# Performance work log

Hardware: AMD Instinct MI355X
Metric: run time of the kernel (lower is better)

## Reference

```python
import math
import jax, jax.numpy as jnp
import numpy as np

B, N, D_FULL, M, D_V = 8, 4096, 256, 256, 256


def _phi(x, omega):
    # x: [..., N, d_full], omega: [M, d_full] -> [..., N, M]
    proj = x @ omega.T
    log_phi = proj - 0.5 * jnp.sum(x * x, axis=-1, keepdims=True)
    log_phi = log_phi - jnp.max(log_phi, axis=-1, keepdims=True)
    return jnp.exp(log_phi) / math.sqrt(omega.shape[0])


def _causal(phi_q, phi_k, V):
    # phi_q/phi_k: [B, N, M], V: [B, N, d_v]
    b, n, m = phi_q.shape
    d_v = V.shape[-1]

    def step(carry, inp):
        S, z = carry
        pq, pk, v = inp  # [B,M], [B,M], [B,d_v]
        S = S + pk[:, :, None] * v[:, None, :]          # [B, M, d_v]
        z = z + pk                                       # [B, M]
        num = jnp.einsum('bi,bij->bj', pq, S)            # [B, d_v]
        den = jnp.maximum(jnp.sum(pq * z, axis=-1), 1e-6)
        return (S, z), num / den[:, None]

    S0 = jnp.zeros((b, m, d_v), phi_q.dtype)
    z0 = jnp.zeros((b, m), phi_q.dtype)
    xs = (jnp.swapaxes(phi_q, 0, 1), jnp.swapaxes(phi_k, 0, 1), jnp.swapaxes(V, 0, 1))
    _, ys = jax.lax.scan(step, (S0, z0), xs)  # ys: [N, B, d_v]
    return jnp.swapaxes(ys, 0, 1)


def setup_inputs() -> dict:
    key = jax.random.key(0)
    kq, kk, kv, ko = jax.random.split(key, 4)
    Q = jax.random.normal(kq, (B, N, D_FULL), dtype=jnp.float32)
    K_in = jax.random.normal(kk, (B, N, D_FULL), dtype=jnp.float32)
    V = jax.random.normal(kv, (B, N, D_V), dtype=jnp.float32)
    omega = jax.random.normal(ko, (M, D_FULL), dtype=jnp.float32)
    return {"Q": Q, "K_in": K_in, "V": V, "omega": omega, "causal": 1}


def reference(Q, K_in, V, omega, causal):
    phi_q = _phi(Q, omega)
    phi_k = _phi(K_in, omega)
    if causal:
        return _causal(phi_q, phi_k, V)
    S = jnp.einsum('bni,bnj->bij', phi_k, V)          # [B, M, d_v]
    z = jnp.sum(phi_k, axis=-2)                        # [B, M]
    num = jnp.einsum('bni,bij->bnj', phi_q, S)
    den = jnp.maximum(jnp.einsum('bni,bi->bn', phi_q, z), 1e-6)
    return num / den[..., None]
```

## Files before the change

### kernel.cpp

```cpp
#include <hip/hip_runtime.h>

#define BN 8
#define NN 4096
#define DD 256
#define MM 256
#define DV 256
#define CHUNK 256
#define NC (NN / CHUNK)

using f32x4 = __attribute__((ext_vector_type(4))) float;
using s16x8 = __attribute__((ext_vector_type(8))) short;

#define MFMA16(a, b, c) __builtin_amdgcn_mfma_f32_16x16x32_bf16(a, b, c, 0, 0, 0)

__device__ __forceinline__ unsigned short f2bf(float x) {
    union { float f; unsigned int u; } v; v.f = x;
    unsigned int r = v.u + 0x7FFF + ((v.u >> 16) & 1);
    return (unsigned short)(r >> 16);
}
__device__ __forceinline__ float bf2f(unsigned short u) {
    union { unsigned int u; float f; } v; v.u = ((unsigned int)u) << 16;
    return v.f;
}

__global__ __launch_bounds__(256) void omconv(
    const float* __restrict__ Om, unsigned short* __restrict__ OmH,
    unsigned short* __restrict__ OmL)
{
    const int i = blockIdx.x * 256 + threadIdx.x;
    const float4 v = *(const float4*)(Om + (size_t)i * 4);
    const float xs[4] = {v.x, v.y, v.z, v.w};
    unsigned short h[4], l[4];
#pragma unroll
    for (int j = 0; j < 4; ++j) {
        h[j] = f2bf(xs[j]);
        l[j] = f2bf(xs[j] - bf2f(h[j]));
    }
    *(uint2*)(OmH + (size_t)i * 4) = *(uint2*)h;
    *(uint2*)(OmL + (size_t)i * 4) = *(uint2*)l;
}

template<bool KPATH>
__global__ __launch_bounds__(256) void phi_mfma(
    const float* __restrict__ X, const unsigned short* __restrict__ OmH,
    const unsigned short* __restrict__ OmL, unsigned short* __restrict__ Phi,
    unsigned short* __restrict__ PhiT, float* __restrict__ Zp)
{
    const int tid = threadIdx.x;
    const int w = tid >> 6;
    const int lane = tid & 63;
    const int col = lane & 15, quad = lane >> 4;
    const long r0 = (long)blockIdx.x * 64;

    __shared__ __align__(16) char lds[67584];
    __shared__ float rowmax_s[64];
    short (*Xh)[264] = (short(*)[264])lds;
    short (*Xl)[264] = (short(*)[264])(lds + 33792);
    unsigned short (*P)[264] = (unsigned short(*)[264])lds;
    unsigned int* P32 = (unsigned int*)lds;
    float (*red)[67] = (float(*)[67])(lds + 34048);

    float4 xv[16];
#pragma unroll
    for (int i = 0; i < 16; ++i)
        xv[i] = *(const float4*)(X + r0 * DD + (size_t)(i * 256 + tid) * 4);
#pragma unroll
    for (int i = 0; i < 16; ++i) {
        const int f = i * 256 + tid;
        const int row = f >> 6;
        const int k4 = (f & 63) * 4;
        const float xs[4] = {xv[i].x, xv[i].y, xv[i].z, xv[i].w};
        unsigned short hh[4], ll[4];
#pragma unroll
        for (int j = 0; j < 4; ++j) {
            hh[j] = f2bf(xs[j]);
            ll[j] = f2bf(xs[j] - bf2f(hh[j]));
        }
        *(uint2*)&Xh[row][k4] = *(uint2*)hh;
        *(uint2*)&Xl[row][k4] = *(uint2*)ll;
    }
    __syncthreads();

    f32x4 acc[4][4] = {};
    s16x8 bh0[4], bl0[4], bh1[4], bl1[4];
#pragma unroll
    for (int ct = 0; ct < 4; ++ct) {
        const size_t off = (size_t)(w * 64 + ct * 16 + col) * DD + quad * 8;
        bh0[ct] = *(const s16x8*)(OmH + off);
        bl0[ct] = *(const s16x8*)(OmL + off);
    }
#pragma unroll
    for (int kt = 0; kt < 8; ++kt) {
        if (kt < 7) {
#pragma unroll
            for (int ct = 0; ct < 4; ++ct) {
                const size_t off = (size_t)(w * 64 + ct * 16 + col) * DD + (kt + 1) * 32 + quad * 8;
                bh1[ct] = *(const s16x8*)(OmH + off);
                bl1[ct] = *(const s16x8*)(OmL + off);
            }
        }
        s16x8 ah[4], al[4];
#pragma unroll
        for (int t = 0; t < 4; ++t) {
            ah[t] = *(const s16x8*)&Xh[t * 16 + col][kt * 32 + quad * 8];
            al[t] = *(const s16x8*)&Xl[t * 16 + col][kt * 32 + quad * 8];
        }
#pragma unroll
        for (int t = 0; t < 4; ++t)
#pragma unroll
            for (int ct = 0; ct < 4; ++ct) {
                acc[t][ct] = MFMA16(ah[t], bh0[ct], acc[t][ct]);
                acc[t][ct] = MFMA16(ah[t], bl0[ct], acc[t][ct]);
                acc[t][ct] = MFMA16(al[t], bh0[ct], acc[t][ct]);
            }
#pragma unroll
        for (int ct = 0; ct < 4; ++ct) { bh0[ct] = bh1[ct]; bl0[ct] = bl1[ct]; }
    }

    __syncthreads();
#pragma unroll
    for (int t = 0; t < 4; ++t)
#pragma unroll
        for (int r = 0; r < 4; ++r) {
            float m = acc[t][0][r];
#pragma unroll
            for (int ct = 1; ct < 4; ++ct) m = fmaxf(m, acc[t][ct][r]);
            red[t * 16 + quad * 4 + r][w * 16 + col] = m;
        }
    __syncthreads();
    if (tid < 64) {
        float m = red[tid][0];
#pragma unroll
        for (int j = 1; j < 64; ++j) m = fmaxf(m, red[tid][j]);
        rowmax_s[tid] = m;
    }
    __syncthreads();

#pragma unroll
    for (int t = 0; t < 4; ++t)
#pragma unroll
        for (int r = 0; r < 4; ++r) {
            const int n = t * 16 + quad * 4 + r;
            const float rm = rowmax_s[n];
#pragma unroll
            for (int ct = 0; ct < 4; ++ct) {
                const float val = __expf(acc[t][ct][r] - rm) * 0.0625f;
                const unsigned u = (unsigned)f2bf(val);
                const unsigned up = (unsigned)__shfl_xor((int)u, 1);
                if ((col & 1) == 0)
                    P32[n * 132 + w * 32 + ct * 8 + (col >> 1)] = u | (up << 16);
            }
        }
    __syncthreads();

    {
        const int t7 = tid & 7;
        const int nb = tid >> 3;
#pragma unroll
        for (int p2 = 0; p2 < 2; ++p2) {
            const int n = p2 * 32 + nb;
#pragma unroll
            for (int s = 0; s < 4; ++s)
                *(uint4*)(Phi + (r0 + n) * MM + t7 * 8 + s * 64) =
                    *(const uint4*)&P[n][t7 * 8 + s * 64];
        }
    }

    if (KPATH) {
        const int b = blockIdx.x >> 6;
        const int c = (blockIdx.x >> 2) & 15;
        const int n0 = (int)(r0 & (NN - 1));
        const int m0 = tid & 31;
        const int nsub = tid >> 5;
#pragma unroll
        for (int mi = 0; mi < 8; ++mi) {
            const int m = mi * 32 + m0;
            unsigned short u[8];
#pragma unroll
            for (int j = 0; j < 8; ++j) u[j] = P[nsub * 8 + j][m];
            *(uint4*)(PhiT + ((size_t)b * MM + m) * NN + n0 + nsub * 8) = *(uint4*)u;
        }
        float z = 0.f;
#pragma unroll
        for (int n = 0; n < 64; ++n) z += bf2f(P[n][tid]);
        atomicAdd(&Zp[((b * NC + c) << 8) + tid], z);
    }
}

__global__ __launch_bounds__(256) void transpose_v(
    const float* __restrict__ V, unsigned short* __restrict__ VT)
{
    const int tid = threadIdx.x;
    const int ct = blockIdx.x & 3;
    const long r0 = (long)(blockIdx.x >> 2) * 64;
    const int b = (int)(r0 >> 12);
    const int n0 = (int)(r0 & (NN - 1));
    __shared__ unsigned short T[64][72];
    const int rr = tid >> 4, cs = tid & 15;
#pragma unroll
    for (int p = 0; p < 4; ++p) {
        const int r = p * 16 + rr;
        const float4 v = *(const float4*)(V + (r0 + r) * DV + ct * 64 + cs * 4);
        T[cs * 4 + 0][r] = f2bf(v.x); T[cs * 4 + 1][r] = f2bf(v.y);
        T[cs * 4 + 2][r] = f2bf(v.z); T[cs * 4 + 3][r] = f2bf(v.w);
    }
    __syncthreads();
    const int cl = tid >> 3, ns = tid & 7;
#pragma unroll
    for (int p = 0; p < 2; ++p) {
        const int c = p * 32 + cl;
        *(uint4*)(VT + ((size_t)b * DV + ct * 64 + c) * NN + n0 + ns * 8) = *(uint4*)&T[c][ns * 8];
    }
}

__global__ __launch_bounds__(256, 3) void state_mfma(
    const unsigned short* __restrict__ VT, const unsigned short* __restrict__ PkT,
    unsigned short* __restrict__ ST)
{
    const int tid = threadIdx.x;
    const int w = tid >> 6;
    const int lane = tid & 63;
    const int col = lane & 15, quad = lane >> 4;
    const int q  = blockIdx.x >> 7;
    const int bc = blockIdx.x & 127;
    const int c  = bc & 15;
    const int b  = bc >> 4;
    const int dv0 = (q & 1) * 128 + (w & 1) * 64;
    const int m0  = (q >> 1) * 128 + (w >> 1) * 64;
    const unsigned short* Ab = VT  + (size_t)b * DV * NN + (size_t)c * CHUNK;
    const unsigned short* Bb = PkT + (size_t)b * MM * NN + (size_t)c * CHUNK;

    f32x4 acc[4][4] = {};
    s16x8 a0[4], b0[4], a1[4], b1[4];
#pragma unroll
    for (int t = 0; t < 4; ++t) {
        a0[t] = *(const s16x8*)(Ab + (size_t)(dv0 + t * 16 + col) * NN + quad * 8);
        b0[t] = *(const s16x8*)(Bb + (size_t)(m0 + t * 16 + col) * NN + quad * 8);
    }
#pragma unroll
    for (int kt = 0; kt < 8; ++kt) {
        if (kt < 7) {
#pragma unroll
            for (int t = 0; t < 4; ++t) {
                a1[t] = *(const s16x8*)(Ab + (size_t)(dv0 + t * 16 + col) * NN + (kt + 1) * 32 + quad * 8);
                b1[t] = *(const s16x8*)(Bb + (size_t)(m0 + t * 16 + col) * NN + (kt + 1) * 32 + quad * 8);
            }
        }
#pragma unroll
        for (int i = 0; i < 4; ++i)
#pragma unroll
            for (int j = 0; j < 4; ++j) acc[i][j] = MFMA16(a0[i], b0[j], acc[i][j]);
#pragma unroll
        for (int t = 0; t < 4; ++t) { a0[t] = a1[t]; b0[t] = b1[t]; }
    }
    unsigned short* Sb = ST + (((size_t)(b * NC + c)) << 16);
#pragma unroll
    for (int i = 0; i < 4; ++i)
#pragma unroll
        for (int j = 0; j < 4; ++j)
#pragma unroll
            for (int r = 0; r < 4; ++r)
                Sb[(dv0 + i * 16 + quad * 4 + r) * MM + m0 + j * 16 + col] = f2bf(acc[i][j][r]);
}

__global__ __launch_bounds__(256) void prefix2(
    unsigned short* __restrict__ ST, float* __restrict__ Z)
{
    const long idx = (long)blockIdx.x * 256 + threadIdx.x;
    const int b = (int)(idx >> 16);
    const int r = (int)(idx & 65535);
    float run = 0.f;
#pragma unroll
    for (int c = 0; c < NC; ++c) {
        const size_t off = (((size_t)(b * NC + c)) << 16) + r;
        const float v = bf2f(ST[off]);
        ST[off] = f2bf(run);
        run += v;
    }
    if (idx < BN * MM) {
        const int b2 = (int)(idx >> 8);
        const int m = (int)(idx & 255);
        float rz = 0.f;
#pragma unroll
        for (int c = 0; c < NC; ++c) {
            const size_t off = (size_t)(b2 * NC + c) * MM + m;
            const float v = Z[off];
            Z[off] = rz;
            rz += v;
        }
    }
}

__global__ __launch_bounds__(256) void out_mfma(
    const unsigned short* __restrict__ PhiQ, const unsigned short* __restrict__ PhiK,
    const unsigned short* __restrict__ VT, const unsigned short* __restrict__ ST,
    const float* __restrict__ Z, float* __restrict__ Out)
{
    const int tid = threadIdx.x;
    const int w = tid >> 6;
    const int lane = tid & 63;
    const int col = lane & 15, quad = lane >> 4;
    const int it = 3 - (blockIdx.x >> 7);
    const int low = blockIdx.x & 127;
    const int c  = low & 15;
    const int b  = low >> 4;
    const size_t chunk_row = (size_t)b * NN + (size_t)c * CHUNK;
    const unsigned short* Qrow = PhiQ + (chunk_row + it * 64) * MM;

    __shared__ unsigned short Qs[64][264];
    __shared__ unsigned short A_s[64][72];
    __shared__ float red[64][68];
    __shared__ float z_s[256];
    __shared__ float den_s[64];

    const float zval = Z[((size_t)(b * NC + c) << 8) + tid];
    s16x8 bk0[8], bk1[8];
#pragma unroll
    for (int ms = 0; ms < 8; ++ms)
        bk0[ms] = *(const s16x8*)(PhiK + (chunk_row)*MM + (size_t)(w * 16 + col) * MM + ms * 32 + quad * 8);
    uint4 qv[8];
#pragma unroll
    for (int i = 0; i < 8; ++i)
        qv[i] = *((const uint4*)Qrow + i * 256 + tid);
    z_s[tid] = zval;
#pragma unroll
    for (int i = 0; i < 8; ++i) {
        const int f = i * 256 + tid;
        *(uint4*)&Qs[f >> 5][(f & 31) * 8] = qv[i];
    }
    __syncthreads();

    f32x4 oacc[4][4] = {};
    float rsum[4][4] = {};

    for (int jt = 0; jt <= it; ++jt) {
        s16x8 bv[8];
        const unsigned short* Vbase = VT + ((size_t)b * DV + w * 64) * NN + (size_t)c * CHUNK + jt * 64;
#pragma unroll
        for (int ks2 = 0; ks2 < 2; ++ks2)
#pragma unroll
            for (int t2 = 0; t2 < 4; ++t2)
                bv[ks2 * 4 + t2] = *(const s16x8*)(Vbase + (size_t)(t2 * 16 + col) * NN + ks2 * 32 + quad * 8);
        f32x4 accA[4] = {};
#pragma unroll
        for (int ms = 0; ms < 8; ++ms)
#pragma unroll
            for (int t = 0; t < 4; ++t) {
                const s16x8 aq = *(const s16x8*)&Qs[t * 16 + col][ms * 32 + quad * 8];
                accA[t] = MFMA16(aq, bk0[ms], accA[t]);
            }
        if (jt < it) {
            const unsigned short* Krn = PhiK + (chunk_row + (jt + 1) * 64) * MM;
#pragma unroll
            for (int ms = 0; ms < 8; ++ms)
                bk1[ms] = *(const s16x8*)(Krn + (size_t)(w * 16 + col) * MM + ms * 32 + quad * 8);
        }
        __syncthreads();
#pragma unroll
        for (int t = 0; t < 4; ++t)
#pragma unroll
            for (int r = 0; r < 4; ++r) {
                const int i_loc = t * 16 + quad * 4 + r;
                const int j_loc = w * 16 + col;
                float v = (jt * 64 + j_loc <= it * 64 + i_loc) ? accA[t][r] : 0.f;
                rsum[t][r] += v;
                A_s[i_loc][j_loc] = f2bf(v);
            }
        __syncthreads();
#pragma unroll
        for (int ks2 = 0; ks2 < 2; ++ks2) {
            s16x8 av[4];
#pragma unroll
            for (int t = 0; t < 4; ++t)
                av[t] = *(const s16x8*)&A_s[t * 16 + col][ks2 * 32 + quad * 8];
#pragma unroll
            for (int t2 = 0; t2 < 4; ++t2)
#pragma unroll
                for (int t = 0; t < 4; ++t)
                    oacc[t][t2] = MFMA16(av[t], bv[ks2 * 4 + t2], oacc[t][t2]);
        }
#pragma unroll
        for (int ms = 0; ms < 8; ++ms) bk0[ms] = bk1[ms];
    }
#pragma unroll
    for (int t = 0; t < 4; ++t)
#pragma unroll
        for (int r = 0; r < 4; ++r)
            red[t * 16 + quad * 4 + r][w * 16 + col] = rsum[t][r];

    const unsigned short* Sb = ST + (((size_t)(b * NC + c)) << 16) + (size_t)(w * 64) * MM;
    s16x8 bs0[4], bs1[4];
#pragma unroll
    for (int t2 = 0; t2 < 4; ++t2)
        bs0[t2] = *(const s16x8*)(Sb + (size_t)(t2 * 16 + col) * MM + quad * 8);
#pragma unroll
    for (int ms = 0; ms < 8; ++ms) {
        if (ms < 7) {
#pragma unroll
            for (int t2 = 0; t2 < 4; ++t2)
                bs1[t2] = *(const s16x8*)(Sb + (size_t)(t2 * 16 + col) * MM + (ms + 1) * 32 + quad * 8);
        }
        s16x8 aq[4];
#pragma unroll
        for (int t = 0; t < 4; ++t)
            aq[t] = *(const s16x8*)&Qs[t * 16 + col][ms * 32 + quad * 8];
#pragma unroll
        for (int t2 = 0; t2 < 4; ++t2)
#pragma unroll
            for (int t = 0; t < 4; ++t)
                oacc[t][t2] = MFMA16(aq[t], bs0[t2], oacc[t][t2]);
#pragma unroll
        for (int t2 = 0; t2 < 4; ++t2) bs0[t2] = bs1[t2];
    }
    {
        const int i = tid & 63;
        const int seg = tid >> 6;
        float d = 0.f;
#pragma unroll
        for (int g = 0; g < 8; ++g) {
            const s16x8 qv8 = *(const s16x8*)&Qs[i][seg * 64 + g * 8];
#pragma unroll
            for (int x = 0; x < 8; ++x)
                d = fmaf(bf2f((unsigned short)qv8[x]), z_s[seg * 64 + g * 8 + x], d);
        }
        red[i][64 + seg] = d;
    }
    __syncthreads();
    if (tid < 64) {
        float s = 0.f;
#pragma unroll
        for (int j = 0; j < 68; ++j) s += red[tid][j];
        den_s[tid] = fmaxf(s, 1e-6f);
    }
    __syncthreads();
#pragma unroll
    for (int t = 0; t < 4; ++t)
#pragma unroll
        for (int r = 0; r < 4; ++r) {
            const int i_loc = t * 16 + quad * 4 + r;
            const float invd = 1.0f / den_s[i_loc];
#pragma unroll
            for (int t2 = 0; t2 < 4; ++t2)
                Out[(chunk_row + it * 64 + i_loc) * DV + w * 64 + t2 * 16 + col] = oacc[t][t2][r] * invd;
        }
}

extern "C" void kernel_launch(void* const* d_in, const int* in_sizes, int n_in,
                              void* d_out, int out_size, void* d_ws, size_t ws_size,
                              hipStream_t stream)
{
    const float* Q  = (const float*)d_in[0];
    const float* K  = (const float*)d_in[1];
    const float* V  = (const float*)d_in[2];
    const float* Om = (const float*)d_in[3];
    float* out = (float*)d_out;

    const size_t NM = (size_t)BN * NN * MM;
    unsigned short* PhiQ  = (unsigned short*)d_ws;
    unsigned short* PhiK  = PhiQ + NM;
    unsigned short* PhiKT = PhiK + NM;
    unsigned short* VT    = PhiKT + NM;
    unsigned short* ST    = VT + NM;
    unsigned short* OmH   = ST + (size_t)BN * NC * DV * MM;
    unsigned short* OmL   = OmH + (size_t)MM * DD;
    float* Z = (float*)(OmL + (size_t)MM * DD);

    hipMemsetAsync(Z, 0, (size_t)BN * NC * MM * sizeof(float), stream);
    omconv<<<dim3(64), dim3(256), 0, stream>>>(Om, OmH, OmL);
    phi_mfma<false><<<dim3((BN * NN) / 64), dim3(256), 0, stream>>>(Q, OmH, OmL, PhiQ, nullptr, nullptr);
    phi_mfma<true><<<dim3((BN * NN) / 64), dim3(256), 0, stream>>>(K, OmH, OmL, PhiK, PhiKT, Z);
    transpose_v<<<dim3((BN * NN) / 64 * 4), dim3(256), 0, stream>>>(V, VT);
    state_mfma<<<dim3(BN * NC * 4), dim3(256), 0, stream>>>(VT, PhiKT, ST);
    prefix2<<<dim3((BN * DV * MM) / 256), dim3(256), 0, stream>>>(ST, Z);
    out_mfma<<<dim3(BN * NC * 4), dim3(256), 0, stream>>>(PhiQ, PhiK, VT, ST, Z, out);
}
```

Before: 253.6 us.

## Fuse Q/K phi kernels and stage fp32 X via direct global-to-LDS loads

Merges the two phi kernel launches into one 1024-block grid, with K blocks first, so there is one launch and the grid is fuller. X rows now go from global memory straight into LDS as fp32 using global_load_lds, in place of register-staged bf16 hi/lo arrays. The hi/lo split happens per MFMA operand at use time, and the hi part is taken by truncation rather than rounding. This cuts register pressure and the LDS store pass, but adds split ALU work inside the inner loop. The truncated hi part slightly changes the split, though the lo term compensates.

```diff
diff --git a/kernel.cpp b/kernel.cpp
--- a/kernel.cpp
+++ b/kernel.cpp
@@ -23,6 +23,20 @@
     return v.f;
 }
 
+__device__ __forceinline__ void split8(const float4 xa, const float4 xb,
+                                       s16x8& ah, s16x8& al)
+{
+    const float xs[8] = {xa.x, xa.y, xa.z, xa.w, xb.x, xb.y, xb.z, xb.w};
+#pragma unroll
+    for (int j = 0; j < 8; ++j) {
+        union { float f; unsigned u; } v; v.f = xs[j];
+        const unsigned hm = v.u & 0xFFFF0000u;
+        union { unsigned u; float f; } hv; hv.u = hm;
+        ah[j] = (short)(hm >> 16);
+        al[j] = (short)f2bf(xs[j] - hv.f);
+    }
+}
+
 __global__ __launch_bounds__(256) void omconv(
     const float* __restrict__ Om, unsigned short* __restrict__ OmH,
     unsigned short* __restrict__ OmL)
@@ -40,44 +54,39 @@
     *(uint2*)(OmL + (size_t)i * 4) = *(uint2*)l;
 }
 
-template<bool KPATH>
-__global__ __launch_bounds__(256) void phi_mfma(
-    const float* __restrict__ X, const unsigned short* __restrict__ OmH,
-    const unsigned short* __restrict__ OmL, unsigned short* __restrict__ Phi,
+__global__ __launch_bounds__(256) void phi_fused(
+    const float* __restrict__ Qp, const float* __restrict__ Kp,
+    const unsigned short* __restrict__ OmH, const unsigned short* __restrict__ OmL,
+    unsigned short* __restrict__ PhiQ, unsigned short* __restrict__ PhiK,
     unsigned short* __restrict__ PhiT, float* __restrict__ Zp)
 {
     const int tid = threadIdx.x;
     const int w = tid >> 6;
     const int lane = tid & 63;
     const int col = lane & 15, quad = lane >> 4;
-    const long r0 = (long)blockIdx.x * 64;
-
-    __shared__ __align__(16) char lds[67584];
+    const bool kpath = blockIdx.x < 512;
+    const int id = kpath ? blockIdx.x : (blockIdx.x - 512);
+    const float* __restrict__ X = kpath ? Kp : Qp;
+    unsigned short* __restrict__ Phi = kpath ? PhiK : PhiQ;
+    const long r0 = (long)id * 64;
+
+    __shared__ __align__(16) char lds[66560];
     __shared__ float rowmax_s[64];
-    short (*Xh)[264] = (short(*)[264])lds;
-    short (*Xl)[264] = (short(*)[264])(lds + 33792);
+    float (*Xs)[260] = (float(*)[260])lds;
     unsigned short (*P)[264] = (unsigned short(*)[264])lds;
     unsigned int* P32 = (unsigned int*)lds;
     float (*red)[67] = (float(*)[67])(lds + 34048);
 
-    float4 xv[16];
-#pragma unroll
-    for (int i = 0; i < 16; ++i)
-        xv[i] = *(const float4*)(X + r0 * DD + (size_t)(i * 256 + tid) * 4);
-#pragma unroll
-    for (int i = 0; i < 16; ++i) {
-        const int f = i * 256 + tid;
-        const int row = f >> 6;
-        const int k4 = (f & 63) * 4;
-        const float xs[4] = {xv[i].x, xv[i].y, xv[i].z, xv[i].w};
-        unsigned short hh[4], ll[4];
-#pragma unroll
-        for (int j = 0; j < 4; ++j) {
-            hh[j] = f2bf(xs[j]);
-            ll[j] = f2bf(xs[j] - bf2f(hh[j]));
-        }
-        *(uint2*)&Xh[row][k4] = *(uint2*)hh;
-        *(uint2*)&Xl[row][k4] = *(uint2*)ll;
+    {
+        const float* gbase = X + r0 * DD + (size_t)lane * 4;
+#pragma unroll
+        for (int j = 0; j < 16; ++j) {
+            const int row = w * 16 + j;
+            __builtin_amdgcn_global_load_lds(
+                (const __attribute__((address_space(1))) unsigned int*)(gbase + (size_t)row * DD),
+                (__attribute__((address_space(3))) unsigned int*)(&Xs[row][0]),
+                16, 0, 0);
+        }
     }
     __syncthreads();
 
@@ -99,20 +108,19 @@
                 bl1[ct] = *(const s16x8*)(OmL + off);
             }
         }
-        s16x8 ah[4], al[4];
 #pragma unroll
         for (int t = 0; t < 4; ++t) {
-            ah[t] = *(const s16x8*)&Xh[t * 16 + col][kt * 32 + quad * 8];
-            al[t] = *(const s16x8*)&Xl[t * 16 + col][kt * 32 + quad * 8];
-        }
-#pragma unroll
-        for (int t = 0; t < 4; ++t)
+            const float4 xa = *(const float4*)&Xs[t * 16 + col][kt * 32 + quad * 8];
+            const float4 xb = *(const float4*)&Xs[t * 16 + col][kt * 32 + quad * 8 + 4];
+            s16x8 ah, al;
+            split8(xa, xb, ah, al);
 #pragma unroll
             for (int ct = 0; ct < 4; ++ct) {
-                acc[t][ct] = MFMA16(ah[t], bh0[ct], acc[t][ct]);
-                acc[t][ct] = MFMA16(ah[t], bl0[ct], acc[t][ct]);
-                acc[t][ct] = MFMA16(al[t], bh0[ct], acc[t][ct]);
-            }
+                acc[t][ct] = MFMA16(ah, bh0[ct], acc[t][ct]);
+                acc[t][ct] = MFMA16(ah, bl0[ct], acc[t][ct]);
+                acc[t][ct] = MFMA16(al, bh0[ct], acc[t][ct]);
+            }
+        }
 #pragma unroll
         for (int ct = 0; ct < 4; ++ct) { bh0[ct] = bh1[ct]; bl0[ct] = bl1[ct]; }
     }
@@ -166,9 +174,9 @@
         }
     }
 
-    if (KPATH) {
-        const int b = blockIdx.x >> 6;
-        const int c = (blockIdx.x >> 2) & 15;
+    if (kpath) {
+        const int b = id >> 6;
+        const int c = (id >> 2) & 15;
         const int n0 = (int)(r0 & (NN - 1));
         const int m0 = tid & 31;
         const int nsub = tid >> 5;
@@ -467,8 +475,7 @@
 
     hipMemsetAsync(Z, 0, (size_t)BN * NC * MM * sizeof(float), stream);
     omconv<<<dim3(64), dim3(256), 0, stream>>>(Om, OmH, OmL);
-    phi_mfma<false><<<dim3((BN * NN) / 64), dim3(256), 0, stream>>>(Q, OmH, OmL, PhiQ, nullptr, nullptr);
-    phi_mfma<true><<<dim3((BN * NN) / 64), dim3(256), 0, stream>>>(K, OmH, OmL, PhiK, PhiKT, Z);
+    phi_fused<<<dim3(1024), dim3(256), 0, stream>>>(Q, K, OmH, OmL, PhiQ, PhiK, PhiKT, Z);
     transpose_v<<<dim3((BN * NN) / 64 * 4), dim3(256), 0, stream>>>(V, VT);
     state_mfma<<<dim3(BN * NC * 4), dim3(256), 0, stream>>>(VT, PhiKT, ST);
     prefix2<<<dim3((BN * DV * MM) / 256), dim3(256), 0, stream>>>(ST, Z);
```

Result: faster. 245.8 us (-3.1%).
